# Performance work log

Hardware: AMD Instinct MI355X
Metric: run time of the kernel (lower is better)

The kernel has to match this reference:

```python
import jax, jax.numpy as jnp
import numpy as np

NUM_GROUPS = 8
EPS = 1e-6

def group_norm(x, gamma, beta):
    # x: [B, C, L]
    B, C, L = x.shape
    g = x.reshape(B, NUM_GROUPS, (C // NUM_GROUPS) * L)
    mean = g.mean(axis=-1, keepdims=True)
    var = g.var(axis=-1, keepdims=True)
    g = (g - mean) * jax.lax.rsqrt(var + EPS)
    g = g.reshape(B, C, L)
    return g * gamma[None, :, None] + beta[None, :, None]

def conv1x1(h, w, b):
    # w: [O, C], b: [O]; h: [B, C, L]
    return jnp.einsum('oc,bcl->bol', w, h) + b[None, :, None]

def setup_inputs() -> dict:
    key = jax.random.key(0)
    ks = jax.random.split(key, 12)
    B, C, L = 8, 512, 2048
    s = 1.0 / np.sqrt(C)
    inp = {
        'x': jax.random.normal(ks[0], (B, C, L), dtype=jnp.float32),
        'gamma': jnp.ones((C,), jnp.float32),
        'beta': jnp.zeros((C,), jnp.float32),
        'wq': jax.random.uniform(ks[1], (C, C), jnp.float32, -s, s),
        'bq': jax.random.uniform(ks[2], (C,), jnp.float32, -s, s),
        'wk': jax.random.uniform(ks[3], (C, C), jnp.float32, -s, s),
        'bk': jax.random.uniform(ks[4], (C,), jnp.float32, -s, s),
        'wv': jax.random.uniform(ks[5], (C, C), jnp.float32, -s, s),
        'bv': jax.random.uniform(ks[6], (C,), jnp.float32, -s, s),
        'wo': jax.random.uniform(ks[7], (C, C), jnp.float32, -s, s),
        'bo': jax.random.uniform(ks[8], (C,), jnp.float32, -s, s),
    }
    return inp

def reference(x, gamma, beta, wq, bq, wk, bk, wv, bv, wo, bo):
    C = x.shape[1]
    h = group_norm(x, gamma, beta)
    q = conv1x1(h, wq, bq)  # [B, C, L]
    k = conv1x1(h, wk, bk)
    v = conv1x1(h, wv, bv)
    # scores: [B, Lq, Lk] = q^T k, scaled by C^-0.5
    w = jnp.einsum('bci,bcj->bij', q, k) * (C ** -0.5)
    w = jax.nn.softmax(w, axis=2)
    # h[b,c,i] = sum_j v[b,c,j] * w[b,i,j]
    h = jnp.einsum('bcj,bij->bci', v, w)
    h = conv1x1(h, wo, bo)
    return x + h
```

## Files before the change

### kernel.cpp

```cpp
#include <hip/hip_runtime.h>
#include <hip/hip_bf16.h>
#include <cstdio>

typedef __attribute__((ext_vector_type(8))) short short8;
typedef __attribute__((ext_vector_type(8))) unsigned short ushort8;
typedef __attribute__((ext_vector_type(4))) float f32x4;
typedef __attribute__((ext_vector_type(4))) unsigned short ushort4v;

__device__ inline unsigned short f2bf(float f){
    unsigned int u = __float_as_uint(f);
    unsigned int r = (u + 0x7fffu + ((u >> 16) & 1u)) >> 16;
    return (unsigned short)r;
}
__device__ inline float bf2f(unsigned short b){
    return __uint_as_float((unsigned int)b << 16);
}

__device__ inline void store1(float* p, float v){ *p = v; }
__device__ inline void store1(unsigned short* p, float v){ *p = f2bf(v); }

#define GLDS(gp, lp) __builtin_amdgcn_global_load_lds( \
    (const __attribute__((address_space(1))) void*)(gp), \
    (__attribute__((address_space(3))) void*)(lp), 16, 0, 0)

#define WAITV(N) asm volatile("s_waitcnt vmcnt(" #N ")" ::: "memory")

#define MFMA_Q(ACC, AF, BF) \
    _Pragma("unroll") \
    for (int ks = 0; ks < 2; ks++) \
        _Pragma("unroll") \
        for (int mi = 0; mi < 4; mi++) \
            _Pragma("unroll") \
            for (int ni = 0; ni < 2; ni++) \
                ACC[mi * 2 + ni] = __builtin_amdgcn_mfma_f32_16x16x32_bf16( \
                    AF[ks][mi], BF[ks][ni], ACC[mi * 2 + ni], 0, 0, 0);

template<typename OutT, int EPI>
__global__ __launch_bounds__(512, 2)
void gemm256(const unsigned short* __restrict__ Ag,
             const unsigned short* __restrict__ Bg,
             OutT* __restrict__ Cg,
             int K, int lda, int ldb, int ldc,
             long sA, long sB, long sC,
             const float* __restrict__ bias,
             float* __restrict__ rs, long sRS,
             float scale)
{
    const int gx = gridDim.x, gy = gridDim.y;
    const int nwg  = gx * gy * (int)gridDim.z;
    const int orig = blockIdx.x + gx * (blockIdx.y + gy * blockIdx.z);
    const int cpx  = nwg >> 3;
    const int nid  = (orig & 7) * cpx + (orig >> 3);
    const int bx   = nid % gx;
    const int tmp  = nid / gx;
    const int by   = tmp % gy;
    const int bz   = tmp / gy;

    Ag += (long)bz * sA;
    Bg += (long)bz * sB;
    Cg += (long)bz * sC;
    const int m0 = by * 256;
    const int n0 = bx * 256;

    __shared__ unsigned short As[2][16384];
    __shared__ unsigned short Bs[2][16384];

    const int t    = threadIdx.x;
    const int wave = t >> 6;
    const int lane = t & 63;
    const int rg   = wave >> 2;
    const int cg   = wave & 3;
    const int wm   = rg * 128;
    const int wn   = cg * 64;
    const int lhi  = lane >> 4;
    const int llo  = lane & 15;

    f32x4 acc0[8], acc1[8], acc2[8], acc3[8];
#pragma unroll
    for (int f = 0; f < 8; f++){
        acc0[f] = (f32x4)(0.0f); acc1[f] = (f32x4)(0.0f);
        acc2[f] = (f32x4)(0.0f); acc3[f] = (f32x4)(0.0f);
    }

    const int s_rr = t >> 3, s_cb = t & 7;
    const int s_cs = s_cb ^ (s_rr & 7);
    auto stageA = [&](int bi, int k0, int j){
        GLDS(Ag + (long)(m0 + j * 64 + s_rr) * lda + k0 + s_cs * 8,
             &As[bi][j * 4096 + wave * 512]);
    };
    auto stageB = [&](int bi, int k0, int j){
        GLDS(Bg + (long)(n0 + j * 64 + s_rr) * ldb + k0 + s_cs * 8,
             &Bs[bi][j * 4096 + wave * 512]);
    };

    const int nt = K >> 6;
    stageB(0, 0, 0); stageB(0, 0, 1); stageB(0, 0, 2); stageB(0, 0, 3);
    stageA(0, 0, 0); stageA(0, 0, 2); stageA(0, 0, 1); stageA(0, 0, 3);
    WAITV(2);
    __builtin_amdgcn_s_barrier();
    __builtin_amdgcn_sched_barrier(0);

    int cur = 0;
    for (int kt = 0; kt < nt; kt++){
        const bool more = (kt + 1 < nt);
        const int nk0 = (kt + 1) << 6;
        short8 af[2][4], bf0[2][2], bf1[2][2];

#pragma unroll
        for (int ks = 0; ks < 2; ks++){
#pragma unroll
            for (int mi = 0; mi < 4; mi++){
                const int r  = wm + mi * 16 + llo;
                const int pc = (ks * 4 + lhi) ^ (r & 7);
                af[ks][mi] = *(const short8*)(&As[cur][r * 64 + pc * 8]);
            }
#pragma unroll
            for (int ni = 0; ni < 2; ni++){
                const int r  = wn + ni * 16 + llo;
                const int pc = (ks * 4 + lhi) ^ (r & 7);
                bf0[ks][ni] = *(const short8*)(&Bs[cur][r * 64 + pc * 8]);
            }
        }
        __builtin_amdgcn_sched_barrier(0);
        if (more){ stageB(cur ^ 1, nk0, 0); stageB(cur ^ 1, nk0, 1); }
        __builtin_amdgcn_s_barrier();
        __builtin_amdgcn_sched_barrier(0);
        __builtin_amdgcn_s_setprio(1);
        MFMA_Q(acc0, af, bf0);
        __builtin_amdgcn_s_setprio(0);
        __builtin_amdgcn_s_barrier();
        __builtin_amdgcn_sched_barrier(0);

#pragma unroll
        for (int ks = 0; ks < 2; ks++)
#pragma unroll
            for (int ni = 0; ni < 2; ni++){
                const int r  = wn + 32 + ni * 16 + llo;
                const int pc = (ks * 4 + lhi) ^ (r & 7);
                bf1[ks][ni] = *(const short8*)(&Bs[cur][r * 64 + pc * 8]);
            }
        __builtin_amdgcn_sched_barrier(0);
        if (more){ stageB(cur ^ 1, nk0, 2); stageB(cur ^ 1, nk0, 3); WAITV(4); }
        else     { WAITV(0); }
        __builtin_amdgcn_s_barrier();
        __builtin_amdgcn_sched_barrier(0);
        __builtin_amdgcn_s_setprio(1);
        MFMA_Q(acc1, af, bf1);
        __builtin_amdgcn_s_setprio(0);
        __builtin_amdgcn_s_barrier();
        __builtin_amdgcn_sched_barrier(0);

#pragma unroll
        for (int ks = 0; ks < 2; ks++)
#pragma unroll
            for (int mi = 0; mi < 4; mi++){
                const int r  = wm + 64 + mi * 16 + llo;
                const int pc = (ks * 4 + lhi) ^ (r & 7);
                af[ks][mi] = *(const short8*)(&As[cur][r * 64 + pc * 8]);
            }
        __builtin_amdgcn_sched_barrier(0);
        if (more){ stageA(cur ^ 1, nk0, 0); stageA(cur ^ 1, nk0, 2); }
        __builtin_amdgcn_s_barrier();
        __builtin_amdgcn_sched_barrier(0);
        __builtin_amdgcn_s_setprio(1);
        MFMA_Q(acc2, af, bf1);
        __builtin_amdgcn_s_setprio(0);
        __builtin_amdgcn_s_barrier();
        __builtin_amdgcn_sched_barrier(0);

        if (more){ stageA(cur ^ 1, nk0, 1); stageA(cur ^ 1, nk0, 3); WAITV(2); }
        __builtin_amdgcn_s_barrier();
        __builtin_amdgcn_sched_barrier(0);
        __builtin_amdgcn_s_setprio(1);
        MFMA_Q(acc3, af, bf0);
        __builtin_amdgcn_s_setprio(0);
        __builtin_amdgcn_s_barrier();
        __builtin_amdgcn_sched_barrier(0);

        cur ^= 1;
    }

    if constexpr (EPI == 4){
        float rp[2][4][4];
#pragma unroll
        for (int h = 0; h < 2; h++)
#pragma unroll
            for (int mi = 0; mi < 4; mi++)
#pragma unroll
                for (int j = 0; j < 4; j++) rp[h][mi][j] = 0.0f;

        auto epi4 = [&](f32x4 (&A)[8], int h, int cl){
#pragma unroll
            for (int mi = 0; mi < 4; mi++)
#pragma unroll
                for (int ni = 0; ni < 2; ni++){
                    const int n  = n0 + wn + cl * 32 + ni * 16 + llo;
                    const int mb = m0 + wm + h * 64 + mi * 16 + lhi * 4;
                    f32x4 v = A[mi * 2 + ni];
#pragma unroll
                    for (int j = 0; j < 4; j++){
                        float e = __expf(v[j] * scale);
                        unsigned short b = f2bf(e);
                        Cg[(long)(mb + j) * ldc + n] = b;
                        rp[h][mi][j] += bf2f(b);
                    }
                }
        };
        epi4(acc0, 0, 0); epi4(acc1, 0, 1); epi4(acc2, 1, 1); epi4(acc3, 1, 0);

#pragma unroll
        for (int h = 0; h < 2; h++)
#pragma unroll
            for (int mi = 0; mi < 4; mi++)
#pragma unroll
                for (int j = 0; j < 4; j++){
                    float v = rp[h][mi][j];
                    v += __shfl_xor(v, 1);
                    v += __shfl_xor(v, 2);
                    v += __shfl_xor(v, 4);
                    v += __shfl_xor(v, 8);
                    rp[h][mi][j] = v;
                }
        __syncthreads();
        float* LDSr = (float*)&As[0][0];
        if (llo == 0){
#pragma unroll
            for (int h = 0; h < 2; h++)
#pragma unroll
                for (int mi = 0; mi < 4; mi++)
#pragma unroll
                    for (int j = 0; j < 4; j++)
                        LDSr[(rg * 128 + h * 64 + mi * 16 + lhi * 4 + j) * 4 + cg]
                            = rp[h][mi][j];
        }
        __syncthreads();
        if (t < 256){
            float s = (LDSr[t * 4 + 0] + LDSr[t * 4 + 1])
                    + (LDSr[t * 4 + 2] + LDSr[t * 4 + 3]);
            atomicAdd(&rs[(long)bz * sRS + m0 + t], s);
        }
    } else {
        auto epi = [&](f32x4 (&A)[8], int h, int cl){
#pragma unroll
            for (int mi = 0; mi < 4; mi++)
#pragma unroll
                for (int ni = 0; ni < 2; ni++){
                    const int n  = n0 + wn + cl * 32 + ni * 16 + llo;
                    const int mb = m0 + wm + h * 64 + mi * 16 + lhi * 4;
                    f32x4 v = A[mi * 2 + ni];
#pragma unroll
                    for (int j = 0; j < 4; j++){
                        float val = v[j] * scale;
                        if (EPI == 1) val += bias[n];
                        store1(&Cg[(long)(mb + j) * ldc + n], val);
                    }
                }
        };
        epi(acc0, 0, 0); epi(acc1, 0, 1); epi(acc2, 1, 1); epi(acc3, 1, 0);
    }
}

template<typename OutT, int EPI>
__global__ __launch_bounds__(256)
void gemm_nt(const unsigned short* __restrict__ Ag,
             const unsigned short* __restrict__ Bg,
             OutT* __restrict__ Cg,
             int K, int lda, int ldb, int ldc,
             long sA, long sB, long sC,
             const float* __restrict__ bias,
             const float* __restrict__ resid, long sR,
             const float* __restrict__ rs, long sRS,
             float scale)
{
    const int gx = gridDim.x, gy = gridDim.y;
    const int nwg  = gx * gy * (int)gridDim.z;
    const int orig = blockIdx.x + gx * (blockIdx.y + gy * blockIdx.z);
    const int cpx  = nwg >> 3;
    const int nid  = (orig & 7) * cpx + (orig >> 3);
    const int bx   = nid % gx;
    const int tmp  = nid / gx;
    const int by   = tmp % gy;
    const int bz   = tmp / gy;

    Ag += (long)bz * sA;
    Bg += (long)bz * sB;
    Cg += (long)bz * sC;
    const int m0 = by * 128;
    const int n0 = bx * 128;

    __shared__ unsigned short As[2][128 * 64];
    __shared__ unsigned short Bs[2][128 * 64];

    const int t    = threadIdx.x;
    const int wave = t >> 6;
    const int lane = t & 63;
    const int wm   = (wave >> 1) << 6;
    const int wn   = (wave & 1) << 6;
    const int lhi  = lane >> 4;
    const int llo  = lane & 15;

    f32x4 acc[4][4];
#pragma unroll
    for (int i = 0; i < 4; i++)
#pragma unroll
        for (int j = 0; j < 4; j++) acc[i][j] = (f32x4)(0.0f);

    auto stage = [&](int bi, int k0){
#pragma unroll
        for (int i = 0; i < 4; i++){
            const int tt = i * 256 + t;
            const int r  = tt >> 3;
            const int cb = tt & 7;
            const int cs = cb ^ (r & 7);
            GLDS(Ag + (long)(m0 + r) * lda + k0 + cs * 8, &As[bi][i * 2048 + wave * 512]);
            GLDS(Bg + (long)(n0 + r) * ldb + k0 + cs * 8, &Bs[bi][i * 2048 + wave * 512]);
        }
    };

    const int nt = K >> 6;
    stage(0, 0);
    __syncthreads();

    int cur = 0;
    for (int kt = 0; kt < nt; kt++){
        if (kt + 1 < nt) stage(cur ^ 1, (kt + 1) << 6);
#pragma unroll
        for (int ksub = 0; ksub < 2; ksub++){
            short8 af[4], bf[4];
#pragma unroll
            for (int mi = 0; mi < 4; mi++){
                const int r  = wm + mi * 16 + llo;
                const int cs = (ksub * 4 + lhi) ^ (r & 7);
                af[mi] = *(const short8*)(&As[cur][r * 64 + cs * 8]);
            }
#pragma unroll
            for (int ni = 0; ni < 4; ni++){
                const int r  = wn + ni * 16 + llo;
                const int cs = (ksub * 4 + lhi) ^ (r & 7);
                bf[ni] = *(const short8*)(&Bs[cur][r * 64 + cs * 8]);
            }
#pragma unroll
            for (int mi = 0; mi < 4; mi++)
#pragma unroll
                for (int ni = 0; ni < 4; ni++)
                    acc[mi][ni] = __builtin_amdgcn_mfma_f32_16x16x32_bf16(
                        af[mi], bf[ni], acc[mi][ni], 0, 0, 0);
        }
        __syncthreads();
        cur ^= 1;
    }

#pragma unroll
    for (int mi = 0; mi < 4; mi++){
#pragma unroll
        for (int ni = 0; ni < 4; ni++){
            const int n  = n0 + wn + ni * 16 + llo;
            const int mb = m0 + wm + mi * 16 + lhi * 4;
            f32x4 v = acc[mi][ni];
#pragma unroll
            for (int j = 0; j < 4; j++){
                const int m = mb + j;
                float val = v[j] * scale;
                if (EPI == 1) val += bias[n];
                if (EPI == 2) val += bias[m];
                if (EPI == 3) val += bias[m] + resid[(long)bz * sR + (long)m * ldc + n];
                if (EPI == 5) val /= rs[(long)bz * sRS + m];
                store1(&Cg[(long)m * ldc + n], val);
            }
        }
    }
}


__global__ void gn_partial(const float* __restrict__ x, float* __restrict__ part){
    const long base = (long)blockIdx.x * 8192;
    const float4* xp = (const float4*)(x + base);
    float s = 0.f, ss = 0.f;
    for (int i = threadIdx.x; i < 2048; i += 256){
        float4 v = xp[i];
        s  += (v.x + v.y) + (v.z + v.w);
        ss += (v.x * v.x + v.y * v.y) + (v.z * v.z + v.w * v.w);
    }
    for (int o = 32; o; o >>= 1){ s += __shfl_down(s, o); ss += __shfl_down(ss, o); }
    __shared__ float rsd[4], rss[4];
    const int wave = threadIdx.x >> 6, lane = threadIdx.x & 63;
    if (lane == 0){ rsd[wave] = s; rss[wave] = ss; }
    __syncthreads();
    if (threadIdx.x == 0){
        part[blockIdx.x * 2]     = (rsd[0] + rsd[1]) + (rsd[2] + rsd[3]);
        part[blockIdx.x * 2 + 1] = (rss[0] + rss[1]) + (rss[2] + rss[3]);
    }
}

__global__ void gn_final(const float* __restrict__ part, float* __restrict__ stats){
    const int bg = threadIdx.x;
    if (bg >= 64) return;
    float s = 0.f, ss = 0.f;
    for (int c = 0; c < 16; c++){
        s  += part[(bg * 16 + c) * 2];
        ss += part[(bg * 16 + c) * 2 + 1];
    }
    const float inv_n = 1.0f / 131072.0f;
    const float mean = s * inv_n;
    const float var  = ss * inv_n - mean * mean;
    stats[bg * 2]     = mean;
    stats[bg * 2 + 1] = rsqrtf(var + 1e-6f);
}

__global__ void norm_transpose(const float* __restrict__ x, const float* __restrict__ stats,
                               const float* __restrict__ gamma, const float* __restrict__ beta,
                               unsigned short* __restrict__ ht){
    const int b = blockIdx.z, c0 = blockIdx.y * 64, l0 = blockIdx.x * 64;
    const int bg = b * 8 + (c0 >> 6);
    const float mean = stats[bg * 2], rstd = stats[bg * 2 + 1];
    __shared__ unsigned short tile[64][66];
    const float* xb = x + (long)b * 1048576;
    const int t = threadIdx.x;
#pragma unroll
    for (int i = 0; i < 16; i++){
        const int idx = i * 256 + t;
        const int c = idx >> 6, l = idx & 63;
        float v = xb[(long)(c0 + c) * 2048 + l0 + l];
        v = (v - mean) * rstd * gamma[c0 + c] + beta[c0 + c];
        tile[l][c] = f2bf(v);
    }
    __syncthreads();
    unsigned short* htb = ht + (long)b * 1048576;
#pragma unroll
    for (int i = 0; i < 16; i++){
        const int idx = i * 256 + t;
        const int l = idx >> 6, c = idx & 63;
        htb[(long)(l0 + l) * 512 + c0 + c] = tile[l][c];
    }
}

__global__ void weights_to_bf16(const float4* __restrict__ wq, const float4* __restrict__ wk,
                                const float4* __restrict__ wv, const float4* __restrict__ wo,
                                const float* __restrict__ bq, const float* __restrict__ bk,
                                ushort4v* __restrict__ out, float* __restrict__ bqk){
    const int i = blockIdx.x * 256 + threadIdx.x;
    if (i < 262144){
        const int w = i >> 16, off = i & 65535;
        const float4* src = (w == 0) ? wq : (w == 1) ? wk : (w == 2) ? wv : wo;
        float4 v = src[off];
        ushort4v o;
        o.x = f2bf(v.x); o.y = f2bf(v.y); o.z = f2bf(v.z); o.w = f2bf(v.w);
        out[i] = o;
    } else {
        const int j = i - 262144;
        if (j < 1024) bqk[j] = (j < 512) ? bq[j] : bk[j - 512];
    }
}

enum : long {
    OFF_WQ  = 0,
    OFF_BQK = 2097152,
    OFF_RS  = OFF_BQK + 4096,
    OFF_HT  = OFF_RS  + 65536,
    OFF_QK  = OFF_HT  + 16777216,
    OFF_V   = OFF_QK  + 33554432,
    OFF_H2  = OFF_V   + 16777216,
    OFF_P   = OFF_H2  + 16777216,
    OFF_GNP = OFF_P   + 67108864,
    OFF_GNS = OFF_GNP + 8192,
    OFF_END = OFF_GNS + 512
};

extern "C" void kernel_launch(void* const* d_in, const int* in_sizes, int n_in,
                              void* d_out, int out_size, void* d_ws, size_t ws_size,
                              hipStream_t stream)
{
    const float* x     = (const float*)d_in[0];
    const float* gamma = (const float*)d_in[1];
    const float* beta  = (const float*)d_in[2];
    const float* wq    = (const float*)d_in[3];
    const float* bq    = (const float*)d_in[4];
    const float* wk    = (const float*)d_in[5];
    const float* bk    = (const float*)d_in[6];
    const float* wv    = (const float*)d_in[7];
    const float* bv    = (const float*)d_in[8];
    const float* wo    = (const float*)d_in[9];
    const float* bo    = (const float*)d_in[10];
    float* out = (float*)d_out;
    char* ws = (char*)d_ws;

    if (ws_size < (size_t)OFF_END){
        fprintf(stderr, "kernel_launch: ws too small (%zu < %ld)\n", ws_size, (long)OFF_END);
        return;
    }

    unsigned short* WQb = (unsigned short*)(ws + OFF_WQ);
    unsigned short* WVb = WQb + 2 * 262144;
    unsigned short* WOb = WQb + 3 * 262144;
    float*          BQK = (float*)(ws + OFF_BQK);
    float*          RS  = (float*)(ws + OFF_RS);
    unsigned short* HT  = (unsigned short*)(ws + OFF_HT);
    unsigned short* QK  = (unsigned short*)(ws + OFF_QK);
    unsigned short* V   = (unsigned short*)(ws + OFF_V);
    unsigned short* H2  = (unsigned short*)(ws + OFF_H2);
    unsigned short* P   = (unsigned short*)(ws + OFF_P);
    float*          GNP = (float*)(ws + OFF_GNP);
    float*          GNS = (float*)(ws + OFF_GNS);

    const long LC  = 1048576;
    const long LQK = 2097152;
    const long LL  = 4194304;

    hipMemsetAsync(RS, 0, 65536, stream);

    weights_to_bf16<<<1028, 256, 0, stream>>>(
        (const float4*)wq, (const float4*)wk, (const float4*)wv, (const float4*)wo,
        bq, bk, (ushort4v*)WQb, BQK);

    gn_partial<<<1024, 256, 0, stream>>>(x, GNP);
    gn_final<<<1, 64, 0, stream>>>(GNP, GNS);
    norm_transpose<<<dim3(32, 8, 8), 256, 0, stream>>>(x, GNS, gamma, beta, HT);

    gemm_nt<unsigned short, 1><<<dim3(8, 16, 8), 256, 0, stream>>>(
        HT, WQb, QK, 512, 512, 512, 1024, LC, 0, LQK, BQK, nullptr, 0, nullptr, 0, 1.0f);
    gemm_nt<unsigned short, 2><<<dim3(16, 4, 8), 256, 0, stream>>>(
        WVb, HT, V, 512, 512, 512, 2048, 0, LC, LC, bv, nullptr, 0, nullptr, 0, 1.0f);

    gemm256<unsigned short, 4><<<dim3(8, 8, 8), 512, 0, stream>>>(
        QK, QK + 512, P, 512, 1024, 1024, 2048, LQK, LQK, LL,
        nullptr, RS, 2048, 0.04419417382f);

    gemm_nt<unsigned short, 5><<<dim3(4, 16, 8), 256, 0, stream>>>(
        P, V, H2, 2048, 2048, 2048, 512, LL, LC, LC, nullptr, nullptr, 0, RS, 2048, 1.0f);

    gemm_nt<float, 3><<<dim3(16, 4, 8), 256, 0, stream>>>(
        WOb, H2, out, 512, 512, 512, 2048, 0, LC, LC, bo, x, LC, nullptr, 0, 1.0f);
}
```

Measured before the change: 270.0 us.

## Drop memset and gn_final launch, replace row-sum atomics with partial buffers

Removes the memset of the softmax row-sum buffer by having each column-block of the score GEMM write its partial row sums to a separate slot, which the PV GEMM then reduces and inverts once per row, turning a per-element divide into a multiply. Folds the group-norm finalisation into norm_transpose, so the single-block gn_final launch goes away. Switches the fused QK projection to the larger gemm256 kernel and accumulates row sums from the unrounded exponentials. The trade-off is a bigger workspace and 8 extra loads per row in the PV epilogue, plus a small numeric difference in the denominator, since the sum no longer uses the bf16-rounded values.

```diff
diff --git a/kernel.cpp b/kernel.cpp
--- a/kernel.cpp
+++ b/kernel.cpp
@@ -200,9 +200,8 @@
 #pragma unroll
                     for (int j = 0; j < 4; j++){
                         float e = __expf(v[j] * scale);
-                        unsigned short b = f2bf(e);
-                        Cg[(long)(mb + j) * ldc + n] = b;
-                        rp[h][mi][j] += bf2f(b);
+                        Cg[(long)(mb + j) * ldc + n] = f2bf(e);
+                        rp[h][mi][j] += e;
                     }
                 }
         };
@@ -237,7 +236,7 @@
         if (t < 256){
             float s = (LDSr[t * 4 + 0] + LDSr[t * 4 + 1])
                     + (LDSr[t * 4 + 2] + LDSr[t * 4 + 3]);
-            atomicAdd(&rs[(long)bz * sRS + m0 + t], s);
+            rs[(long)bz * sRS + (long)bx * 2048 + m0 + t] = s;
         }
     } else {
         auto epi = [&](f32x4 (&A)[8], int h, int cl){
@@ -350,6 +349,21 @@
         cur ^= 1;
     }
 
+    float inv_d[4][4];
+    if constexpr (EPI == 5){
+#pragma unroll
+        for (int mi = 0; mi < 4; mi++)
+#pragma unroll
+            for (int j = 0; j < 4; j++){
+                const int m = m0 + wm + mi * 16 + lhi * 4 + j;
+                float s = 0.f;
+#pragma unroll
+                for (int p = 0; p < 8; p++)
+                    s += rs[(long)bz * sRS + p * 2048 + m];
+                inv_d[mi][j] = 1.0f / s;
+            }
+    }
+
 #pragma unroll
     for (int mi = 0; mi < 4; mi++){
 #pragma unroll
@@ -364,7 +378,7 @@
                 if (EPI == 1) val += bias[n];
                 if (EPI == 2) val += bias[m];
                 if (EPI == 3) val += bias[m] + resid[(long)bz * sR + (long)m * ldc + n];
-                if (EPI == 5) val /= rs[(long)bz * sRS + m];
+                if (EPI == 5) val *= inv_d[mi][j];
                 store1(&Cg[(long)m * ldc + n], val);
             }
         }
@@ -392,30 +406,31 @@
     }
 }
 
-__global__ void gn_final(const float* __restrict__ part, float* __restrict__ stats){
-    const int bg = threadIdx.x;
-    if (bg >= 64) return;
-    float s = 0.f, ss = 0.f;
-    for (int c = 0; c < 16; c++){
-        s  += part[(bg * 16 + c) * 2];
-        ss += part[(bg * 16 + c) * 2 + 1];
-    }
-    const float inv_n = 1.0f / 131072.0f;
-    const float mean = s * inv_n;
-    const float var  = ss * inv_n - mean * mean;
-    stats[bg * 2]     = mean;
-    stats[bg * 2 + 1] = rsqrtf(var + 1e-6f);
-}
-
-__global__ void norm_transpose(const float* __restrict__ x, const float* __restrict__ stats,
+__global__ void norm_transpose(const float* __restrict__ x, const float* __restrict__ part,
                                const float* __restrict__ gamma, const float* __restrict__ beta,
                                unsigned short* __restrict__ ht){
     const int b = blockIdx.z, c0 = blockIdx.y * 64, l0 = blockIdx.x * 64;
     const int bg = b * 8 + (c0 >> 6);
-    const float mean = stats[bg * 2], rstd = stats[bg * 2 + 1];
+    __shared__ float sm[2];
+    const int t = threadIdx.x;
+    if (t < 16){
+        float s  = part[(bg * 16 + t) * 2];
+        float ss = part[(bg * 16 + t) * 2 + 1];
+        s  += __shfl_xor(s, 1);  ss += __shfl_xor(ss, 1);
+        s  += __shfl_xor(s, 2);  ss += __shfl_xor(ss, 2);
+        s  += __shfl_xor(s, 4);  ss += __shfl_xor(ss, 4);
+        s  += __shfl_xor(s, 8);  ss += __shfl_xor(ss, 8);
+        if (t == 0){
+            const float inv_n = 1.0f / 131072.0f;
+            const float mean = s * inv_n;
+            const float var  = ss * inv_n - mean * mean;
+            sm[0] = mean; sm[1] = rsqrtf(var + 1e-6f);
+        }
+    }
+    __syncthreads();
+    const float mean = sm[0], rstd = sm[1];
     __shared__ unsigned short tile[64][66];
     const float* xb = x + (long)b * 1048576;
-    const int t = threadIdx.x;
 #pragma unroll
     for (int i = 0; i < 16; i++){
         const int idx = i * 256 + t;
@@ -456,14 +471,13 @@
     OFF_WQ  = 0,
     OFF_BQK = 2097152,
     OFF_RS  = OFF_BQK + 4096,
-    OFF_HT  = OFF_RS  + 65536,
+    OFF_HT  = OFF_RS  + 524288,
     OFF_QK  = OFF_HT  + 16777216,
     OFF_V   = OFF_QK  + 33554432,
     OFF_H2  = OFF_V   + 16777216,
     OFF_P   = OFF_H2  + 16777216,
     OFF_GNP = OFF_P   + 67108864,
-    OFF_GNS = OFF_GNP + 8192,
-    OFF_END = OFF_GNS + 512
+    OFF_END = OFF_GNP + 8192
 };
 
 extern "C" void kernel_launch(void* const* d_in, const int* in_sizes, int n_in,
@@ -500,33 +514,29 @@
     unsigned short* H2  = (unsigned short*)(ws + OFF_H2);
     unsigned short* P   = (unsigned short*)(ws + OFF_P);
     float*          GNP = (float*)(ws + OFF_GNP);
-    float*          GNS = (float*)(ws + OFF_GNS);
 
     const long LC  = 1048576;
     const long LQK = 2097152;
     const long LL  = 4194304;
 
-    hipMemsetAsync(RS, 0, 65536, stream);
-
     weights_to_bf16<<<1028, 256, 0, stream>>>(
         (const float4*)wq, (const float4*)wk, (const float4*)wv, (const float4*)wo,
         bq, bk, (ushort4v*)WQb, BQK);
 
     gn_partial<<<1024, 256, 0, stream>>>(x, GNP);
-    gn_final<<<1, 64, 0, stream>>>(GNP, GNS);
-    norm_transpose<<<dim3(32, 8, 8), 256, 0, stream>>>(x, GNS, gamma, beta, HT);
-
-    gemm_nt<unsigned short, 1><<<dim3(8, 16, 8), 256, 0, stream>>>(
-        HT, WQb, QK, 512, 512, 512, 1024, LC, 0, LQK, BQK, nullptr, 0, nullptr, 0, 1.0f);
+    norm_transpose<<<dim3(32, 8, 8), 256, 0, stream>>>(x, GNP, gamma, beta, HT);
+
+    gemm256<unsigned short, 1><<<dim3(4, 8, 8), 512, 0, stream>>>(
+        HT, WQb, QK, 512, 512, 512, 1024, LC, 0, LQK, BQK, nullptr, 0, 1.0f);
     gemm_nt<unsigned short, 2><<<dim3(16, 4, 8), 256, 0, stream>>>(
         WVb, HT, V, 512, 512, 512, 2048, 0, LC, LC, bv, nullptr, 0, nullptr, 0, 1.0f);
 
     gemm256<unsigned short, 4><<<dim3(8, 8, 8), 512, 0, stream>>>(
         QK, QK + 512, P, 512, 1024, 1024, 2048, LQK, LQK, LL,
-        nullptr, RS, 2048, 0.04419417382f);
+        nullptr, RS, 16384, 0.04419417382f);
 
     gemm_nt<unsigned short, 5><<<dim3(4, 16, 8), 256, 0, stream>>>(
-        P, V, H2, 2048, 2048, 2048, 512, LL, LC, LC, nullptr, nullptr, 0, RS, 2048, 1.0f);
+        P, V, H2, 2048, 2048, 2048, 512, LL, LC, LC, nullptr, nullptr, 0, RS, 16384, 1.0f);
 
     gemm_nt<float, 3><<<dim3(16, 4, 8), 256, 0, stream>>>(
         WOb, H2, out, 512, 512, 512, 2048, 0, LC, LC, bo, x, LC, nullptr, 0, 1.0f);
```

Result: faster. 254.6 us (-5.7%).
